# Kernel optimization log

Hardware: AMD Instinct MI355X
Metric: run time of the kernel (lower is better)

The kernel has to match this reference:

```python
import jax, jax.numpy as jnp
import numpy as np

N, E = 100000, 1600000
IN, HID, HEADS, OUT = 128, 16, 4, 64
SLOPE = 0.2  # leaky_relu negative_slope default


def setup_inputs() -> dict:
    key = jax.random.key(0)
    ks = jax.random.split(key, 12)
    s = 0.1  # xavier-ish scale
    return {
        "x": jax.random.normal(ks[0], (N, IN), jnp.float32),
        "edge_index": jax.random.randint(ks[1], (2, E), 0, N, jnp.int32),
        "W1": jax.random.normal(ks[2], (IN, HEADS * HID), jnp.float32) * s,
        "att_l1": jax.random.normal(ks[3], (1, HEADS, HID), jnp.float32) * s,
        "att_r1": jax.random.normal(ks[4], (1, HEADS, HID), jnp.float32) * s,
        "res_W1": jax.random.normal(ks[5], (IN, HEADS * HID), jnp.float32) * s,
        "b1": jnp.zeros((HEADS * HID,), jnp.float32),
        "W2": jax.random.normal(ks[6], (HEADS * HID, OUT), jnp.float32) * s,
        "att_l2": jax.random.normal(ks[7], (1, 1, OUT), jnp.float32) * s,
        "att_r2": jax.random.normal(ks[8], (1, 1, OUT), jnp.float32) * s,
        "b2": jnp.zeros((OUT,), jnp.float32),
    }


def agdn_conv(x, W, att_l, att_r, bias, res_W, src, dst):
    # x: [n, in]; W: [in, H*C]; att_*: [1, H, C]
    n = x.shape[0]
    H, C = att_l.shape[1], att_l.shape[2]
    x_lin = (x @ W).reshape(n, H, C)
    # residual: res_fc if present, else identity on x_lin (residual=True path)
    x_res = (x @ res_W) if res_W is not None else x_lin.reshape(n, H * C)
    al = jnp.sum(x_lin * att_l, axis=-1)  # [n, H]
    ar = jnp.sum(x_lin * att_r, axis=-1)  # [n, H]
    logits = jax.nn.leaky_relu(al[src] + ar[dst], SLOPE)  # [E, H]
    # segment softmax over incoming edges of each dst node
    m = jax.ops.segment_max(logits, dst, num_segments=n)
    e = jnp.exp(logits - m[dst])
    ssum = jax.ops.segment_sum(e, dst, num_segments=n)
    alpha = e / (ssum[dst] + 1e-16)  # [E, H]
    msg = x_lin[src] * alpha[:, :, None]  # [E, H, C]
    out = jax.ops.segment_sum(msg, dst, num_segments=n).reshape(n, H * C)
    return out + x_res + bias


def reference(x, edge_index, W1, att_l1, att_r1, res_W1, b1, W2, att_l2, att_r2, b2):
    src, dst = edge_index[0], edge_index[1]
    h = agdn_conv(x, W1, att_l1, att_r1, b1, res_W1, src, dst)
    h = jax.nn.elu(h)
    # last layer: heads=1, in==heads*out so res_fc is None (residual = x_lin)
    return agdn_conv(h, W2, att_l2, att_r2, b2, None, src, dst)
```

## Files before the change

kernel.cpp:

```cpp
#include <hip/hip_runtime.h>
#include <hip/hip_bf16.h>
#include <hip/hip_fp16.h>
#include <math.h>

#define NN 100000
#define EE 1600000
#define IN_DIM 128
#define HID 16
#define HEADS 4
#define D1 64
#define OUT_DIM 64
#define SLOPE 0.2f

#define NB 391
#define BCAP 5120
#define BINA_CHUNK 4096
#define BINA_BLOCKS ((EE + BINA_CHUNK - 1) / BINA_CHUNK)
#define NODE_BLOCKS ((NN + 63) / 64)
#define AGG_BLOCKS (NN / 32)

#define W1COLS 144
#define LDB1 272
#define LDB2 144

typedef __attribute__((ext_vector_type(8))) short bf16x8;
typedef __attribute__((ext_vector_type(4))) float f32x4;

__device__ __forceinline__ float leaky(float v) { return v > 0.f ? v : SLOPE * v; }
__device__ __forceinline__ unsigned short f2bf(float f) {
    __hip_bfloat16 h = __float2bfloat16(f);
    return *(unsigned short*)&h;
}
__device__ __forceinline__ __half2 u2h2(unsigned u) {
    union { unsigned u; __half2 h; } c; c.u = u; return c.h;
}
__device__ __forceinline__ bf16x8 pack8(float4 a, float4 b) {
    bf16x8 r;
    r[0] = (short)f2bf(a.x); r[1] = (short)f2bf(a.y);
    r[2] = (short)f2bf(a.z); r[3] = (short)f2bf(a.w);
    r[4] = (short)f2bf(b.x); r[5] = (short)f2bf(b.y);
    r[6] = (short)f2bf(b.z); r[7] = (short)f2bf(b.w);
    return r;
}

__global__ __launch_bounds__(256, 4) void node1_kernel(
        const float* __restrict__ x,
        const unsigned short* __restrict__ Wtb,
        const float* __restrict__ b1,
        __half* __restrict__ xlin1h,
        __half* __restrict__ acc1h,
        float* __restrict__ al1,
        float* __restrict__ ar1) {
    __shared__ char smemB[W1COLS * LDB1];
    int t = threadIdx.x;
    int base = blockIdx.x * 64;
    int wave = t >> 6, lane = t & 63;
    int quad = lane >> 4, li = lane & 15;
    int node = base + wave * 16 + li;

    uint4 breg[9];
#pragma unroll
    for (int s = 0; s < 9; s++) {
        int seg = s * 256 + t;
        breg[s] = *(const uint4*)(Wtb + (seg >> 4) * 128 + (seg & 15) * 8);
    }
    float4 xreg[8];
#pragma unroll
    for (int i = 0; i < 8; i++) xreg[i] = make_float4(0.f, 0.f, 0.f, 0.f);
    if (node < NN) {
        const float* xp = x + (size_t)node * IN_DIM + quad * 8;
#pragma unroll
        for (int kc = 0; kc < 4; kc++) {
            xreg[kc * 2]     = *(const float4*)(xp + kc * 32);
            xreg[kc * 2 + 1] = *(const float4*)(xp + kc * 32 + 4);
        }
    }
#pragma unroll
    for (int s = 0; s < 9; s++) {
        int seg = s * 256 + t;
        *(uint4*)(smemB + (seg >> 4) * LDB1 + (seg & 15) * 16) = breg[s];
    }
    __syncthreads();

    f32x4 accs[9];
#pragma unroll
    for (int nt = 0; nt < 9; nt++) accs[nt] = (f32x4){0.f, 0.f, 0.f, 0.f};
#pragma unroll
    for (int kc = 0; kc < 4; kc++) {
        bf16x8 afrag = pack8(xreg[kc * 2], xreg[kc * 2 + 1]);
        const char* brow = smemB + kc * 64 + quad * 16;
#pragma unroll
        for (int nt = 0; nt < 9; nt++) {
            bf16x8 bfrag = *(const bf16x8*)(brow + (nt * 16 + li) * LDB1);
            accs[nt] = __builtin_amdgcn_mfma_f32_16x16x32_bf16(afrag, bfrag, accs[nt], 0, 0, 0);
        }
    }

    int m0 = base + wave * 16;
#pragma unroll
    for (int nt = 0; nt < 4; nt++) {
#pragma unroll
        for (int j = 0; j < 4; j++) {
            int nd = m0 + quad * 4 + j;
            if (nd < NN) xlin1h[(size_t)nd * D1 + nt * 16 + li] = __float2half(accs[nt][j]);
        }
    }
#pragma unroll
    for (int nt = 4; nt < 8; nt++) {
        int col = (nt - 4) * 16 + li;
        float bv = b1[col];
#pragma unroll
        for (int j = 0; j < 4; j++) {
            int nd = m0 + quad * 4 + j;
            if (nd < NN) acc1h[(size_t)nd * D1 + col] = __float2half(accs[nt][j] + bv);
        }
    }
#pragma unroll
    for (int j = 0; j < 4; j++) {
        int nd = m0 + quad * 4 + j;
        if (nd < NN) {
            if (li < 4) al1[nd * HEADS + li] = accs[8][j];
            else if (li < 8) ar1[nd * HEADS + (li - 4)] = accs[8][j];
        }
    }
}

__global__ void prep_kernel(int* __restrict__ bucket_cursor,
                            const float* __restrict__ W1,
                            const float* __restrict__ resW,
                            const float* __restrict__ W2,
                            const float* __restrict__ attl1,
                            const float* __restrict__ attr1,
                            const float* __restrict__ attl2,
                            const float* __restrict__ attr2,
                            unsigned short* __restrict__ Wtb,
                            unsigned short* __restrict__ W2tb,
                            float* __restrict__ vl, float* __restrict__ vr) {
    int t = threadIdx.x;
    if (blockIdx.x == 0) {
        if (t < NB) bucket_cursor[t] = t * BCAP;
    } else if (blockIdx.x == 1) {
        for (int idx = t; idx < W1COLS * 128; idx += 512) {
            int col = idx >> 7, k = idx & 127;
            float w = 0.f;
            if (col < 64) {
                w = W1[k * 64 + col];
            } else if (col < 128) {
                w = resW[k * 64 + (col - 64)];
            } else if (col < 132) {
                int hh = col - 128;
                for (int c = 0; c < HID; c++)
                    w += W1[k * 64 + hh * HID + c] * attl1[hh * HID + c];
            } else if (col < 136) {
                int hh = col - 132;
                for (int c = 0; c < HID; c++)
                    w += W1[k * 64 + hh * HID + c] * attr1[hh * HID + c];
            }
            Wtb[idx] = f2bf(w);
        }
    } else {
        for (int idx = t; idx < 64 * 64; idx += 512) {
            int col = idx >> 6, k = idx & 63;
            W2tb[idx] = f2bf(W2[k * 64 + col]);
        }
        if (t < D1) {
            float a = 0.f, b = 0.f;
            for (int o = 0; o < OUT_DIM; o++) {
                float w = W2[t * OUT_DIM + o];
                a += w * attl2[o];
                b += w * attr2[o];
            }
            vl[t] = a; vr[t] = b;
        }
    }
}

__global__ __launch_bounds__(256) void binA_kernel(const int* __restrict__ src,
                                                   const int* __restrict__ dst,
                                                   int* __restrict__ bucket_cursor,
                                                   unsigned* __restrict__ binned) {
    __shared__ unsigned spack[BINA_CHUNK];
    __shared__ unsigned short sbkt[BINA_CHUNK];
    __shared__ int lhist[512], lscan[512], gbase[512], lcur[512];
    int t = threadIdx.x;
    lhist[t] = 0; lhist[t + 256] = 0;
    lcur[t] = 0;  lcur[t + 256] = 0;
    __syncthreads();
    int e0 = blockIdx.x * BINA_CHUNK;
    int nvalid = EE - e0; if (nvalid > BINA_CHUNK) nvalid = BINA_CHUNK;
    unsigned pk[16];
    unsigned short bk[16];
#pragma unroll
    for (int i = 0; i < 16; i++) {
        int e = e0 + t + i * 256;
        if (e < EE) {
            int d = dst[e], s = src[e];
            int b = d >> 8;
            pk[i] = ((unsigned)(d & 255) << 24) | (unsigned)s;
            bk[i] = (unsigned short)b;
            atomicAdd(&lhist[b], 1);
        } else bk[i] = 0xFFFFu;
    }
    __syncthreads();
    int c1 = lhist[t], c2 = lhist[t + 256];
    for (int off = 1; off < 512; off <<= 1) {
        int a1 = (t >= off) ? lhist[t - off] : 0;
        int a2 = (t + 256 >= off) ? lhist[t + 256 - off] : 0;
        __syncthreads();
        lhist[t] += a1; lhist[t + 256] += a2;
        __syncthreads();
    }
    lscan[t] = lhist[t] - c1;
    lscan[t + 256] = lhist[t + 256] - c2;
    if (c1) gbase[t] = atomicAdd(&bucket_cursor[t], c1);
    if (c2) gbase[t + 256] = atomicAdd(&bucket_cursor[t + 256], c2);
    __syncthreads();
#pragma unroll
    for (int i = 0; i < 16; i++) {
        if (bk[i] != 0xFFFFu) {
            int b = bk[i];
            int pos = atomicAdd(&lcur[b], 1);
            int slot = lscan[b] + pos;
            spack[slot] = pk[i];
            sbkt[slot] = (unsigned short)b;
        }
    }
    __syncthreads();
    for (int j = t; j < nvalid; j += 256) {
        int b = sbkt[j];
        int idx = gbase[b] + (j - lscan[b]);
        if (idx < (b + 1) * BCAP) binned[idx] = spack[j];
    }
}

__global__ __launch_bounds__(256) void binB_kernel(const unsigned* __restrict__ binned,
                                                   const int* __restrict__ bucket_cursor,
                                                   int* __restrict__ row_ptr,
                                                   int* __restrict__ counts,
                                                   int* __restrict__ sorted_src) {
    __shared__ int lcount[256], lrow[256], lcur[256];
    int b = blockIdx.x, t = threadIdx.x;
    int start = b * BCAP;
    int cnt = bucket_cursor[b] - start;
    if (cnt > BCAP) cnt = BCAP;
    lcount[t] = 0;
    __syncthreads();
    for (int i = t; i < cnt; i += 256) {
        atomicAdd(&lcount[binned[start + i] >> 24], 1);
    }
    __syncthreads();
    int v = lcount[t];
    lrow[t] = v;
    __syncthreads();
    for (int off = 1; off < 256; off <<= 1) {
        int a = (t >= off) ? lrow[t - off] : 0;
        __syncthreads();
        lrow[t] += a;
        __syncthreads();
    }
    int ex = lrow[t] - v;
    __syncthreads();
    lrow[t] = ex;
    lcur[t] = 0;
    int node = (b << 8) + t;
    if (node < NN) {
        row_ptr[node] = start + ex;
        counts[node] = v;
    }
    __syncthreads();
    for (int i = t; i < cnt; i += 256) {
        unsigned p = binned[start + i];
        int low = p >> 24;
        int pos = atomicAdd(&lcur[low], 1);
        sorted_src[start + lrow[low] + pos] = (int)(p & 0xFFFFFFu);
    }
}

__global__ __launch_bounds__(256) void agg1_kernel(
        const int* __restrict__ sorted_src, const int* __restrict__ row_ptr,
        const int* __restrict__ counts,
        const float* __restrict__ al1, const float* __restrict__ ar1,
        const __half* __restrict__ xlin1h, const __half* __restrict__ acc1h,
        unsigned short* __restrict__ hb,
        const float* __restrict__ vl, const float* __restrict__ vr,
        float* __restrict__ al2, float* __restrict__ ar2) {
    __shared__ __half s_alpha[4][8][65][4];
    __shared__ int    s_src[4][8][65];
    int w = threadIdx.x >> 6, lane = threadIdx.x & 63;
    int g = lane >> 3, li = lane & 7;
    int d = blockIdx.x * 32 + w * 8 + g;
    int rs = row_ptr[d];
    int deg = counts[d];
    const float4 arv = *(const float4*)(ar1 + d * 4);
    int h = li >> 1;

    int maxdeg = deg;
    maxdeg = max(maxdeg, __shfl_xor(maxdeg, 8, 64));
    maxdeg = max(maxdeg, __shfl_xor(maxdeg, 16, 64));
    maxdeg = max(maxdeg, __shfl_xor(maxdeg, 32, 64));
    bool big = maxdeg > 64;

    float s0 = 0.f, s1 = 0.f, s2 = 0.f, s3 = 0.f;
    if (!big) {
#pragma unroll
        for (int it = 0; it < 8; it++) {
            int e = li + it * 8;
            if (e < deg) {
                int s = sorted_src[rs + e];
                const float4 alv = *(const float4*)(al1 + s * 4);
                float e0 = __expf(leaky(alv.x + arv.x));
                float e1 = __expf(leaky(alv.y + arv.y));
                float e2 = __expf(leaky(alv.z + arv.z));
                float e3 = __expf(leaky(alv.w + arv.w));
                s0 += e0; s1 += e1; s2 += e2; s3 += e3;
                __half2 h01 = __floats2half2_rn(e0, e1);
                __half2 h23 = __floats2half2_rn(e2, e3);
                *(uint2*)&s_alpha[w][g][e][0] =
                    make_uint2(*(unsigned*)&h01, *(unsigned*)&h23);
                s_src[w][g][e] = s;
            }
        }
    } else {
        for (int e = li; e < deg; e += 8) {
            int s = sorted_src[rs + e];
            const float4 alv = *(const float4*)(al1 + s * 4);
            s0 += __expf(leaky(alv.x + arv.x));
            s1 += __expf(leaky(alv.y + arv.y));
            s2 += __expf(leaky(alv.z + arv.z));
            s3 += __expf(leaky(alv.w + arv.w));
        }
    }
#pragma unroll
    for (int off = 1; off < 8; off <<= 1) {
        s0 += __shfl_xor(s0, off, 64);
        s1 += __shfl_xor(s1, off, 64);
        s2 += __shfl_xor(s2, off, 64);
        s3 += __shfl_xor(s3, off, 64);
    }
    float inv0 = 0.f, inv1 = 0.f, inv2 = 0.f, inv3 = 0.f;
    if (deg > 0) {
        inv0 = 1.f / (s0 + 1e-16f); inv1 = 1.f / (s1 + 1e-16f);
        inv2 = 1.f / (s2 + 1e-16f); inv3 = 1.f / (s3 + 1e-16f);
    }
    float invh = (h == 0) ? inv0 : (h == 1) ? inv1 : (h == 2) ? inv2 : inv3;
    __half2 invh2 = __floats2half2_rn(invh, invh);

    __half2 a01 = __floats2half2_rn(0.f, 0.f);
    __half2 a23 = a01, a45 = a01, a67 = a01;
    float fb0=0.f, fb1=0.f, fb2=0.f, fb3=0.f, fb4=0.f, fb5=0.f, fb6=0.f, fb7=0.f;
    if (!big) {
        for (int i0 = 0; i0 < maxdeg; i0 += 4) {
            int ss[4]; __half ah[4]; uint4 uu[4];
#pragma unroll
            for (int j = 0; j < 4; j++) {
                int i = i0 + j;
                ah[j] = __float2half(0.f);
                ss[j] = 0;
                if (i < deg) { ss[j] = s_src[w][g][i]; ah[j] = s_alpha[w][g][i][h]; }
            }
#pragma unroll
            for (int j = 0; j < 4; j++) {
                int i = i0 + j;
                uu[j] = make_uint4(0u, 0u, 0u, 0u);
                if (i < deg) uu[j] = *(const uint4*)(xlin1h + (size_t)ss[j] * D1 + li * 8);
            }
#pragma unroll
            for (int j = 0; j < 4; j++) {
                __half2 a2 = __hmul2(__half2half2(ah[j]), invh2);
                a01 = __hfma2(a2, u2h2(uu[j].x), a01);
                a23 = __hfma2(a2, u2h2(uu[j].y), a23);
                a45 = __hfma2(a2, u2h2(uu[j].z), a45);
                a67 = __hfma2(a2, u2h2(uu[j].w), a67);
            }
        }
    } else {
        float arh = (h == 0) ? arv.x : (h == 1) ? arv.y : (h == 2) ? arv.z : arv.w;
        for (int i = 0; i < deg; i++) {
            int s = sorted_src[rs + i];
            const float4 alv = *(const float4*)(al1 + s * 4);
            float lv = (h == 0) ? alv.x : (h == 1) ? alv.y : (h == 2) ? alv.z : alv.w;
            float a = __expf(leaky(lv + arh)) * invh;
            uint4 u = *(const uint4*)(xlin1h + (size_t)s * D1 + li * 8);
            float2 x01 = __half22float2(u2h2(u.x));
            float2 x23 = __half22float2(u2h2(u.y));
            float2 x45 = __half22float2(u2h2(u.z));
            float2 x67 = __half22float2(u2h2(u.w));
            fb0 += a * x01.x; fb1 += a * x01.y; fb2 += a * x23.x; fb3 += a * x23.y;
            fb4 += a * x45.x; fb5 += a * x45.y; fb6 += a * x67.x; fb7 += a * x67.y;
        }
    }
    float c0, c1, c2, c3, c4, c5, c6, c7;
    { float2 tv;
      tv = __half22float2(a01); c0 = tv.x + fb0; c1 = tv.y + fb1;
      tv = __half22float2(a23); c2 = tv.x + fb2; c3 = tv.y + fb3;
      tv = __half22float2(a45); c4 = tv.x + fb4; c5 = tv.y + fb5;
      tv = __half22float2(a67); c6 = tv.x + fb6; c7 = tv.y + fb7; }
    uint4 rres = *(const uint4*)(acc1h + (size_t)d * D1 + li * 8);
    { float2 tv;
      tv = __half22float2(u2h2(rres.x)); c0 += tv.x; c1 += tv.y;
      tv = __half22float2(u2h2(rres.y)); c2 += tv.x; c3 += tv.y;
      tv = __half22float2(u2h2(rres.z)); c4 += tv.x; c5 += tv.y;
      tv = __half22float2(u2h2(rres.w)); c6 += tv.x; c7 += tv.y; }
    c0 = c0 > 0.f ? c0 : (__expf(c0) - 1.f);
    c1 = c1 > 0.f ? c1 : (__expf(c1) - 1.f);
    c2 = c2 > 0.f ? c2 : (__expf(c2) - 1.f);
    c3 = c3 > 0.f ? c3 : (__expf(c3) - 1.f);
    c4 = c4 > 0.f ? c4 : (__expf(c4) - 1.f);
    c5 = c5 > 0.f ? c5 : (__expf(c5) - 1.f);
    c6 = c6 > 0.f ? c6 : (__expf(c6) - 1.f);
    c7 = c7 > 0.f ? c7 : (__expf(c7) - 1.f);
    union { unsigned short us[8]; uint4 u4; } hw;
    hw.us[0] = f2bf(c0); hw.us[1] = f2bf(c1); hw.us[2] = f2bf(c2); hw.us[3] = f2bf(c3);
    hw.us[4] = f2bf(c4); hw.us[5] = f2bf(c5); hw.us[6] = f2bf(c6); hw.us[7] = f2bf(c7);
    *(uint4*)(hb + (size_t)d * D1 + li * 8) = hw.u4;
    const float4 vla = *(const float4*)(vl + li * 8);
    const float4 vlb = *(const float4*)(vl + li * 8 + 4);
    const float4 vra = *(const float4*)(vr + li * 8);
    const float4 vrb = *(const float4*)(vr + li * 8 + 4);
    float pl = c0 * vla.x + c1 * vla.y + c2 * vla.z + c3 * vla.w
             + c4 * vlb.x + c5 * vlb.y + c6 * vlb.z + c7 * vlb.w;
    float pr = c0 * vra.x + c1 * vra.y + c2 * vra.z + c3 * vra.w
             + c4 * vrb.x + c5 * vrb.y + c6 * vrb.z + c7 * vrb.w;
#pragma unroll
    for (int off = 1; off < 8; off <<= 1) {
        pl += __shfl_xor(pl, off, 64);
        pr += __shfl_xor(pr, off, 64);
    }
    if (li == 0) { al2[d] = pl; ar2[d] = pr; }
}

__global__ __launch_bounds__(256) void node2_kernel(
        const unsigned short* __restrict__ hb,
        const unsigned short* __restrict__ W2tb,
        __half* __restrict__ xlin2h) {
    __shared__ char smemB[64 * LDB2];
    int t = threadIdx.x;
    int base = blockIdx.x * 64;
    int wave = t >> 6, lane = t & 63;
    int quad = lane >> 4, li = lane & 15;
    int node = base + wave * 16 + li;

    uint4 breg[2];
#pragma unroll
    for (int s = 0; s < 2; s++) {
        int seg = s * 256 + t;
        breg[s] = *(const uint4*)(W2tb + (seg >> 3) * 64 + (seg & 7) * 8);
    }
    bf16x8 afr[2];
#pragma unroll
    for (int kc = 0; kc < 2; kc++)
#pragma unroll
        for (int i = 0; i < 8; i++) afr[kc][i] = 0;
    if (node < NN) {
        afr[0] = *(const bf16x8*)(hb + (size_t)node * D1 + quad * 8);
        afr[1] = *(const bf16x8*)(hb + (size_t)node * D1 + 32 + quad * 8);
    }
#pragma unroll
    for (int s = 0; s < 2; s++) {
        int seg = s * 256 + t;
        *(uint4*)(smemB + (seg >> 3) * LDB2 + (seg & 7) * 16) = breg[s];
    }
    __syncthreads();

    f32x4 accs[4];
#pragma unroll
    for (int nt = 0; nt < 4; nt++) accs[nt] = (f32x4){0.f, 0.f, 0.f, 0.f};
#pragma unroll
    for (int kc = 0; kc < 2; kc++) {
        const char* brow = smemB + kc * 64 + quad * 16;
#pragma unroll
        for (int nt = 0; nt < 4; nt++) {
            bf16x8 bfrag = *(const bf16x8*)(brow + (nt * 16 + li) * LDB2);
            accs[nt] = __builtin_amdgcn_mfma_f32_16x16x32_bf16(afr[kc], bfrag, accs[nt], 0, 0, 0);
        }
    }

    int m0 = base + wave * 16;
#pragma unroll
    for (int nt = 0; nt < 4; nt++) {
        int col = nt * 16 + li;
#pragma unroll
        for (int j = 0; j < 4; j++) {
            int nd = m0 + quad * 4 + j;
            if (nd < NN) xlin2h[(size_t)nd * OUT_DIM + col] = __float2half(accs[nt][j]);
        }
    }
}

__global__ __launch_bounds__(256) void agg2_kernel(
        const int* __restrict__ sorted_src, const int* __restrict__ row_ptr,
        const int* __restrict__ counts,
        const float* __restrict__ al2, const float* __restrict__ ar2,
        const __half* __restrict__ xlin2h, const float* __restrict__ b2,
        float* __restrict__ out) {
    __shared__ __half s_alpha[4][8][65];
    __shared__ int    s_src[4][8][65];
    int w = threadIdx.x >> 6, lane = threadIdx.x & 63;
    int g = lane >> 3, li = lane & 7;
    int d = blockIdx.x * 32 + w * 8 + g;
    int rs = row_ptr[d];
    int deg = counts[d];
    float ard = ar2[d];

    int maxdeg = deg;
    maxdeg = max(maxdeg, __shfl_xor(maxdeg, 8, 64));
    maxdeg = max(maxdeg, __shfl_xor(maxdeg, 16, 64));
    maxdeg = max(maxdeg, __shfl_xor(maxdeg, 32, 64));
    bool big = maxdeg > 64;

    float ssum = 0.f;
    if (!big) {
#pragma unroll
        for (int it = 0; it < 8; it++) {
            int e = li + it * 8;
            if (e < deg) {
                int s = sorted_src[rs + e];
                float ex = __expf(leaky(al2[s] + ard));
                ssum += ex;
                s_alpha[w][g][e] = __float2half(ex);
                s_src[w][g][e] = s;
            }
        }
    } else {
        for (int e = li; e < deg; e += 8) {
            int s = sorted_src[rs + e];
            ssum += __expf(leaky(al2[s] + ard));
        }
    }
#pragma unroll
    for (int off = 1; off < 8; off <<= 1) ssum += __shfl_xor(ssum, off, 64);
    float inv = (deg > 0) ? 1.f / (ssum + 1e-16f) : 0.f;
    __half2 inv2h = __floats2half2_rn(inv, inv);

    __half2 a01 = __floats2half2_rn(0.f, 0.f);
    __half2 a23 = a01, a45 = a01, a67 = a01;
    float fb0=0.f, fb1=0.f, fb2=0.f, fb3=0.f, fb4=0.f, fb5=0.f, fb6=0.f, fb7=0.f;
    if (!big) {
        for (int i0 = 0; i0 < maxdeg; i0 += 4) {
            int ss[4]; __half ah[4]; uint4 uu[4];
#pragma unroll
            for (int j = 0; j < 4; j++) {
                int i = i0 + j;
                ah[j] = __float2half(0.f);
                ss[j] = 0;
                if (i < deg) { ss[j] = s_src[w][g][i]; ah[j] = s_alpha[w][g][i]; }
            }
#pragma unroll
            for (int j = 0; j < 4; j++) {
                int i = i0 + j;
                uu[j] = make_uint4(0u, 0u, 0u, 0u);
                if (i < deg) uu[j] = *(const uint4*)(xlin2h + (size_t)ss[j] * OUT_DIM + li * 8);
            }
#pragma unroll
            for (int j = 0; j < 4; j++) {
                __half2 a2 = __hmul2(__half2half2(ah[j]), inv2h);
                a01 = __hfma2(a2, u2h2(uu[j].x), a01);
                a23 = __hfma2(a2, u2h2(uu[j].y), a23);
                a45 = __hfma2(a2, u2h2(uu[j].z), a45);
                a67 = __hfma2(a2, u2h2(uu[j].w), a67);
            }
        }
    } else {
        for (int i = 0; i < deg; i++) {
            int s = sorted_src[rs + i];
            float a = __expf(leaky(al2[s] + ard)) * inv;
            uint4 u = *(const uint4*)(xlin2h + (size_t)s * OUT_DIM + li * 8);
            float2 x01 = __half22float2(u2h2(u.x));
            float2 x23 = __half22float2(u2h2(u.y));
            float2 x45 = __half22float2(u2h2(u.z));
            float2 x67 = __half22float2(u2h2(u.w));
            fb0 += a * x01.x; fb1 += a * x01.y; fb2 += a * x23.x; fb3 += a * x23.y;
            fb4 += a * x45.x; fb5 += a * x45.y; fb6 += a * x67.x; fb7 += a * x67.y;
        }
    }
    float c0, c1, c2, c3, c4, c5, c6, c7;
    { float2 tv;
      tv = __half22float2(a01); c0 = tv.x + fb0; c1 = tv.y + fb1;
      tv = __half22float2(a23); c2 = tv.x + fb2; c3 = tv.y + fb3;
      tv = __half22float2(a45); c4 = tv.x + fb4; c5 = tv.y + fb5;
      tv = __half22float2(a67); c6 = tv.x + fb6; c7 = tv.y + fb7; }
    uint4 own = *(const uint4*)(xlin2h + (size_t)d * OUT_DIM + li * 8);
    { float2 tv;
      tv = __half22float2(u2h2(own.x)); c0 += tv.x; c1 += tv.y;
      tv = __half22float2(u2h2(own.y)); c2 += tv.x; c3 += tv.y;
      tv = __half22float2(u2h2(own.z)); c4 += tv.x; c5 += tv.y;
      tv = __half22float2(u2h2(own.w)); c6 += tv.x; c7 += tv.y; }
    const float4 bva = *(const float4*)(b2 + li * 8);
    const float4 bvb = *(const float4*)(b2 + li * 8 + 4);
    c0 += bva.x; c1 += bva.y; c2 += bva.z; c3 += bva.w;
    c4 += bvb.x; c5 += bvb.y; c6 += bvb.z; c7 += bvb.w;
    float* p = out + (size_t)d * OUT_DIM + li * 8;
    *(float4*)p = make_float4(c0, c1, c2, c3);
    *(float4*)(p + 4) = make_float4(c4, c5, c6, c7);
}

extern "C" void kernel_launch(void* const* d_in, const int* in_sizes, int n_in,
                              void* d_out, int out_size, void* d_ws, size_t ws_size,
                              hipStream_t stream) {
    const float* x     = (const float*)d_in[0];
    const int*   eidx  = (const int*)d_in[1];
    const float* W1    = (const float*)d_in[2];
    const float* attl1 = (const float*)d_in[3];
    const float* attr1 = (const float*)d_in[4];
    const float* resW1 = (const float*)d_in[5];
    const float* b1    = (const float*)d_in[6];
    const float* W2    = (const float*)d_in[7];
    const float* attl2 = (const float*)d_in[8];
    const float* attr2 = (const float*)d_in[9];
    const float* b2    = (const float*)d_in[10];

    const int* src = eidx;
    const int* dst = eidx + EE;

    __half* xlin1h = (__half*)d_ws;
    __half* acc1h  = xlin1h + (size_t)NN * D1;
    unsigned short* hb = (unsigned short*)(acc1h + (size_t)NN * D1);
    float* al1   = (float*)(hb + (size_t)NN * D1);
    float* ar1   = al1 + (size_t)NN * HEADS;
    float* al2   = ar1 + (size_t)NN * HEADS;
    float* ar2   = al2 + NN;
    float* vl    = ar2 + NN;
    float* vr    = vl + D1;
    unsigned short* Wtb  = (unsigned short*)(vr + D1);
    unsigned short* W2tb = Wtb + W1COLS * 128;
    int* counts        = (int*)(W2tb + 64 * 64);
    int* row_ptr       = counts + NN;
    int* bucket_cursor = row_ptr + NN;
    int* sorted_src    = bucket_cursor + 512;
    unsigned* binned = (unsigned*)d_out;
    __half* xlin2h = xlin1h;

    float* out = (float*)d_out;

    prep_kernel<<<3, 512, 0, stream>>>(bucket_cursor, W1, resW1, W2,
                                       attl1, attr1, attl2, attr2,
                                       Wtb, W2tb, vl, vr);
    binA_kernel<<<BINA_BLOCKS, 256, 0, stream>>>(src, dst, bucket_cursor, binned);
    node1_kernel<<<NODE_BLOCKS, 256, 0, stream>>>(x, Wtb, b1,
                                                  xlin1h, acc1h, al1, ar1);
    binB_kernel<<<NB, 256, 0, stream>>>(binned, bucket_cursor,
                                        row_ptr, counts, sorted_src);

    agg1_kernel<<<AGG_BLOCKS, 256, 0, stream>>>(sorted_src, row_ptr, counts,
                                                al1, ar1, xlin1h, acc1h, hb,
                                                vl, vr, al2, ar2);

    node2_kernel<<<NODE_BLOCKS, 256, 0, stream>>>(hb, W2tb, xlin2h);
    agg2_kernel<<<AGG_BLOCKS, 256, 0, stream>>>(sorted_src, row_ptr, counts,
                                                al2, ar2, xlin2h, b2, out);
}
```

Before: 258.1 us.

## Aggregate before layer-2 projection, fuse binning with node1, unroll gathers by eight

Layer 2 now aggregates the 64-dim ELU output h directly and applies W2 afterward, using linearity: the sum of alpha·h plus h is multiplied by W2 once per node. The layer-2 attention logits still come from the precomputed vl/vr projections. The binA and node1 kernels are merged into one launch that picks its role by block index, so the two independent stages can overlap. The gather loops in both aggregation kernels are unrolled from 4 to 8 for more memory-level parallelism. This adds an extra rounding step through half/bf16 storage of the aggregated sum, which may change numerics, and the deeper unroll raises register use.

```diff
diff --git a/kernel.cpp b/kernel.cpp
--- a/kernel.cpp
+++ b/kernel.cpp
@@ -41,88 +41,6 @@
     r[4] = (short)f2bf(b.x); r[5] = (short)f2bf(b.y);
     r[6] = (short)f2bf(b.z); r[7] = (short)f2bf(b.w);
     return r;
-}
-
-__global__ __launch_bounds__(256, 4) void node1_kernel(
-        const float* __restrict__ x,
-        const unsigned short* __restrict__ Wtb,
-        const float* __restrict__ b1,
-        __half* __restrict__ xlin1h,
-        __half* __restrict__ acc1h,
-        float* __restrict__ al1,
-        float* __restrict__ ar1) {
-    __shared__ char smemB[W1COLS * LDB1];
-    int t = threadIdx.x;
-    int base = blockIdx.x * 64;
-    int wave = t >> 6, lane = t & 63;
-    int quad = lane >> 4, li = lane & 15;
-    int node = base + wave * 16 + li;
-
-    uint4 breg[9];
-#pragma unroll
-    for (int s = 0; s < 9; s++) {
-        int seg = s * 256 + t;
-        breg[s] = *(const uint4*)(Wtb + (seg >> 4) * 128 + (seg & 15) * 8);
-    }
-    float4 xreg[8];
-#pragma unroll
-    for (int i = 0; i < 8; i++) xreg[i] = make_float4(0.f, 0.f, 0.f, 0.f);
-    if (node < NN) {
-        const float* xp = x + (size_t)node * IN_DIM + quad * 8;
-#pragma unroll
-        for (int kc = 0; kc < 4; kc++) {
-            xreg[kc * 2]     = *(const float4*)(xp + kc * 32);
-            xreg[kc * 2 + 1] = *(const float4*)(xp + kc * 32 + 4);
-        }
-    }
-#pragma unroll
-    for (int s = 0; s < 9; s++) {
-        int seg = s * 256 + t;
-        *(uint4*)(smemB + (seg >> 4) * LDB1 + (seg & 15) * 16) = breg[s];
-    }
-    __syncthreads();
-
-    f32x4 accs[9];
-#pragma unroll
-    for (int nt = 0; nt < 9; nt++) accs[nt] = (f32x4){0.f, 0.f, 0.f, 0.f};
-#pragma unroll
-    for (int kc = 0; kc < 4; kc++) {
-        bf16x8 afrag = pack8(xreg[kc * 2], xreg[kc * 2 + 1]);
-        const char* brow = smemB + kc * 64 + quad * 16;
-#pragma unroll
-        for (int nt = 0; nt < 9; nt++) {
-            bf16x8 bfrag = *(const bf16x8*)(brow + (nt * 16 + li) * LDB1);
-            accs[nt] = __builtin_amdgcn_mfma_f32_16x16x32_bf16(afrag, bfrag, accs[nt], 0, 0, 0);
-        }
-    }
-
-    int m0 = base + wave * 16;
-#pragma unroll
-    for (int nt = 0; nt < 4; nt++) {
-#pragma unroll
-        for (int j = 0; j < 4; j++) {
-            int nd = m0 + quad * 4 + j;
-            if (nd < NN) xlin1h[(size_t)nd * D1 + nt * 16 + li] = __float2half(accs[nt][j]);
-        }
-    }
-#pragma unroll
-    for (int nt = 4; nt < 8; nt++) {
-        int col = (nt - 4) * 16 + li;
-        float bv = b1[col];
-#pragma unroll
-        for (int j = 0; j < 4; j++) {
-            int nd = m0 + quad * 4 + j;
-            if (nd < NN) acc1h[(size_t)nd * D1 + col] = __float2half(accs[nt][j] + bv);
-        }
-    }
-#pragma unroll
-    for (int j = 0; j < 4; j++) {
-        int nd = m0 + quad * 4 + j;
-        if (nd < NN) {
-            if (li < 4) al1[nd * HEADS + li] = accs[8][j];
-            else if (li < 8) ar1[nd * HEADS + (li - 4)] = accs[8][j];
-        }
-    }
 }
 
 __global__ void prep_kernel(int* __restrict__ bucket_cursor,
@@ -175,18 +93,20 @@
     }
 }
 
-__global__ __launch_bounds__(256) void binA_kernel(const int* __restrict__ src,
-                                                   const int* __restrict__ dst,
-                                                   int* __restrict__ bucket_cursor,
-                                                   unsigned* __restrict__ binned) {
-    __shared__ unsigned spack[BINA_CHUNK];
-    __shared__ unsigned short sbkt[BINA_CHUNK];
-    __shared__ int lhist[512], lscan[512], gbase[512], lcur[512];
+__device__ __forceinline__ void binA_body(char* smem, int bid,
+        const int* __restrict__ src, const int* __restrict__ dst,
+        int* __restrict__ bucket_cursor, unsigned* __restrict__ binned) {
+    unsigned* spack = (unsigned*)smem;
+    unsigned short* sbkt = (unsigned short*)(smem + 16384);
+    int* lhist = (int*)(smem + 24576);
+    int* lscan = lhist + 512;
+    int* gbase = lscan + 512;
+    int* lcur  = gbase + 512;
     int t = threadIdx.x;
     lhist[t] = 0; lhist[t + 256] = 0;
     lcur[t] = 0;  lcur[t + 256] = 0;
     __syncthreads();
-    int e0 = blockIdx.x * BINA_CHUNK;
+    int e0 = bid * BINA_CHUNK;
     int nvalid = EE - e0; if (nvalid > BINA_CHUNK) nvalid = BINA_CHUNK;
     unsigned pk[16];
     unsigned short bk[16];
@@ -231,6 +151,98 @@
         int idx = gbase[b] + (j - lscan[b]);
         if (idx < (b + 1) * BCAP) binned[idx] = spack[j];
     }
+}
+
+__device__ __forceinline__ void node1_body(char* smemB, int bid,
+        const float* __restrict__ x, const unsigned short* __restrict__ Wtb,
+        const float* __restrict__ b1, __half* __restrict__ xlin1h,
+        __half* __restrict__ acc1h, float* __restrict__ al1,
+        float* __restrict__ ar1) {
+    int t = threadIdx.x;
+    int base = bid * 64;
+    int wave = t >> 6, lane = t & 63;
+    int quad = lane >> 4, li = lane & 15;
+    int node = base + wave * 16 + li;
+
+    uint4 breg[9];
+#pragma unroll
+    for (int s = 0; s < 9; s++) {
+        int seg = s * 256 + t;
+        breg[s] = *(const uint4*)(Wtb + (seg >> 4) * 128 + (seg & 15) * 8);
+    }
+    float4 xreg[8];
+#pragma unroll
+    for (int i = 0; i < 8; i++) xreg[i] = make_float4(0.f, 0.f, 0.f, 0.f);
+    if (node < NN) {
+        const float* xp = x + (size_t)node * IN_DIM + quad * 8;
+#pragma unroll
+        for (int kc = 0; kc < 4; kc++) {
+            xreg[kc * 2]     = *(const float4*)(xp + kc * 32);
+            xreg[kc * 2 + 1] = *(const float4*)(xp + kc * 32 + 4);
+        }
+    }
+#pragma unroll
+    for (int s = 0; s < 9; s++) {
+        int seg = s * 256 + t;
+        *(uint4*)(smemB + (seg >> 4) * LDB1 + (seg & 15) * 16) = breg[s];
+    }
+    __syncthreads();
+
+    f32x4 accs[9];
+#pragma unroll
+    for (int nt = 0; nt < 9; nt++) accs[nt] = (f32x4){0.f, 0.f, 0.f, 0.f};
+#pragma unroll
+    for (int kc = 0; kc < 4; kc++) {
+        bf16x8 afrag = pack8(xreg[kc * 2], xreg[kc * 2 + 1]);
+        const char* brow = smemB + kc * 64 + quad * 16;
+#pragma unroll
+        for (int nt = 0; nt < 9; nt++) {
+            bf16x8 bfrag = *(const bf16x8*)(brow + (nt * 16 + li) * LDB1);
+            accs[nt] = __builtin_amdgcn_mfma_f32_16x16x32_bf16(afrag, bfrag, accs[nt], 0, 0, 0);
+        }
+    }
+
+    int m0 = base + wave * 16;
+#pragma unroll
+    for (int nt = 0; nt < 4; nt++) {
+#pragma unroll
+        for (int j = 0; j < 4; j++) {
+            int nd = m0 + quad * 4 + j;
+            if (nd < NN) xlin1h[(size_t)nd * D1 + nt * 16 + li] = __float2half(accs[nt][j]);
+        }
+    }
+#pragma unroll
+    for (int nt = 4; nt < 8; nt++) {
+        int col = (nt - 4) * 16 + li;
+        float bv = b1[col];
+#pragma unroll
+        for (int j = 0; j < 4; j++) {
+            int nd = m0 + quad * 4 + j;
+            if (nd < NN) acc1h[(size_t)nd * D1 + col] = __float2half(accs[nt][j] + bv);
+        }
+    }
+#pragma unroll
+    for (int j = 0; j < 4; j++) {
+        int nd = m0 + quad * 4 + j;
+        if (nd < NN) {
+            if (li < 4) al1[nd * HEADS + li] = accs[8][j];
+            else if (li < 8) ar1[nd * HEADS + (li - 4)] = accs[8][j];
+        }
+    }
+}
+
+__global__ __launch_bounds__(256, 4) void fusedA_kernel(
+        const int* __restrict__ src, const int* __restrict__ dst,
+        int* __restrict__ bucket_cursor, unsigned* __restrict__ binned,
+        const float* __restrict__ x, const unsigned short* __restrict__ Wtb,
+        const float* __restrict__ b1, __half* __restrict__ xlin1h,
+        __half* __restrict__ acc1h, float* __restrict__ al1,
+        float* __restrict__ ar1) {
+    __shared__ __align__(16) char smem[W1COLS * LDB1];
+    if (blockIdx.x < BINA_BLOCKS)
+        binA_body(smem, blockIdx.x, src, dst, bucket_cursor, binned);
+    else
+        node1_body(smem, blockIdx.x - BINA_BLOCKS, x, Wtb, b1, xlin1h, acc1h, al1, ar1);
 }
 
 __global__ __launch_bounds__(256) void binB_kernel(const unsigned* __restrict__ binned,
@@ -281,7 +293,7 @@
         const int* __restrict__ counts,
         const float* __restrict__ al1, const float* __restrict__ ar1,
         const __half* __restrict__ xlin1h, const __half* __restrict__ acc1h,
-        unsigned short* __restrict__ hb,
+        __half* __restrict__ hh,
         const float* __restrict__ vl, const float* __restrict__ vr,
         float* __restrict__ al2, float* __restrict__ ar2) {
     __shared__ __half s_alpha[4][8][65][4];
@@ -349,23 +361,23 @@
     __half2 a23 = a01, a45 = a01, a67 = a01;
     float fb0=0.f, fb1=0.f, fb2=0.f, fb3=0.f, fb4=0.f, fb5=0.f, fb6=0.f, fb7=0.f;
     if (!big) {
-        for (int i0 = 0; i0 < maxdeg; i0 += 4) {
-            int ss[4]; __half ah[4]; uint4 uu[4];
-#pragma unroll
-            for (int j = 0; j < 4; j++) {
+        for (int i0 = 0; i0 < maxdeg; i0 += 8) {
+            int ss[8]; __half ah[8]; uint4 uu[8];
+#pragma unroll
+            for (int j = 0; j < 8; j++) {
                 int i = i0 + j;
-                ah[j] = __float2half(0.f);
-                ss[j] = 0;
-                if (i < deg) { ss[j] = s_src[w][g][i]; ah[j] = s_alpha[w][g][i][h]; }
-            }
-#pragma unroll
-            for (int j = 0; j < 4; j++) {
+                bool v = i < deg;
+                ss[j] = v ? s_src[w][g][i] : 0;
+                ah[j] = v ? s_alpha[w][g][i][h] : __float2half(0.f);
+            }
+#pragma unroll
+            for (int j = 0; j < 8; j++) {
                 int i = i0 + j;
                 uu[j] = make_uint4(0u, 0u, 0u, 0u);
                 if (i < deg) uu[j] = *(const uint4*)(xlin1h + (size_t)ss[j] * D1 + li * 8);
             }
 #pragma unroll
-            for (int j = 0; j < 4; j++) {
+            for (int j = 0; j < 8; j++) {
                 __half2 a2 = __hmul2(__half2half2(ah[j]), invh2);
                 a01 = __hfma2(a2, u2h2(uu[j].x), a01);
                 a23 = __hfma2(a2, u2h2(uu[j].y), a23);
@@ -409,10 +421,13 @@
     c5 = c5 > 0.f ? c5 : (__expf(c5) - 1.f);
     c6 = c6 > 0.f ? c6 : (__expf(c6) - 1.f);
     c7 = c7 > 0.f ? c7 : (__expf(c7) - 1.f);
-    union { unsigned short us[8]; uint4 u4; } hw;
-    hw.us[0] = f2bf(c0); hw.us[1] = f2bf(c1); hw.us[2] = f2bf(c2); hw.us[3] = f2bf(c3);
-    hw.us[4] = f2bf(c4); hw.us[5] = f2bf(c5); hw.us[6] = f2bf(c6); hw.us[7] = f2bf(c7);
-    *(uint4*)(hb + (size_t)d * D1 + li * 8) = hw.u4;
+    __half2 o01 = __floats2half2_rn(c0, c1);
+    __half2 o23 = __floats2half2_rn(c2, c3);
+    __half2 o45 = __floats2half2_rn(c4, c5);
+    __half2 o67 = __floats2half2_rn(c6, c7);
+    uint4 hv = make_uint4(*(unsigned*)&o01, *(unsigned*)&o23,
+                          *(unsigned*)&o45, *(unsigned*)&o67);
+    *(uint4*)(hh + (size_t)d * D1 + li * 8) = hv;
     const float4 vla = *(const float4*)(vl + li * 8);
     const float4 vlb = *(const float4*)(vl + li * 8 + 4);
     const float4 vra = *(const float4*)(vr + li * 8);
@@ -429,70 +444,12 @@
     if (li == 0) { al2[d] = pl; ar2[d] = pr; }
 }
 
-__global__ __launch_bounds__(256) void node2_kernel(
-        const unsigned short* __restrict__ hb,
-        const unsigned short* __restrict__ W2tb,
-        __half* __restrict__ xlin2h) {
-    __shared__ char smemB[64 * LDB2];
-    int t = threadIdx.x;
-    int base = blockIdx.x * 64;
-    int wave = t >> 6, lane = t & 63;
-    int quad = lane >> 4, li = lane & 15;
-    int node = base + wave * 16 + li;
-
-    uint4 breg[2];
-#pragma unroll
-    for (int s = 0; s < 2; s++) {
-        int seg = s * 256 + t;
-        breg[s] = *(const uint4*)(W2tb + (seg >> 3) * 64 + (seg & 7) * 8);
-    }
-    bf16x8 afr[2];
-#pragma unroll
-    for (int kc = 0; kc < 2; kc++)
-#pragma unroll
-        for (int i = 0; i < 8; i++) afr[kc][i] = 0;
-    if (node < NN) {
-        afr[0] = *(const bf16x8*)(hb + (size_t)node * D1 + quad * 8);
-        afr[1] = *(const bf16x8*)(hb + (size_t)node * D1 + 32 + quad * 8);
-    }
-#pragma unroll
-    for (int s = 0; s < 2; s++) {
-        int seg = s * 256 + t;
-        *(uint4*)(smemB + (seg >> 3) * LDB2 + (seg & 7) * 16) = breg[s];
-    }
-    __syncthreads();
-
-    f32x4 accs[4];
-#pragma unroll
-    for (int nt = 0; nt < 4; nt++) accs[nt] = (f32x4){0.f, 0.f, 0.f, 0.f};
-#pragma unroll
-    for (int kc = 0; kc < 2; kc++) {
-        const char* brow = smemB + kc * 64 + quad * 16;
-#pragma unroll
-        for (int nt = 0; nt < 4; nt++) {
-            bf16x8 bfrag = *(const bf16x8*)(brow + (nt * 16 + li) * LDB2);
-            accs[nt] = __builtin_amdgcn_mfma_f32_16x16x32_bf16(afr[kc], bfrag, accs[nt], 0, 0, 0);
-        }
-    }
-
-    int m0 = base + wave * 16;
-#pragma unroll
-    for (int nt = 0; nt < 4; nt++) {
-        int col = nt * 16 + li;
-#pragma unroll
-        for (int j = 0; j < 4; j++) {
-            int nd = m0 + quad * 4 + j;
-            if (nd < NN) xlin2h[(size_t)nd * OUT_DIM + col] = __float2half(accs[nt][j]);
-        }
-    }
-}
-
 __global__ __launch_bounds__(256) void agg2_kernel(
         const int* __restrict__ sorted_src, const int* __restrict__ row_ptr,
         const int* __restrict__ counts,
         const float* __restrict__ al2, const float* __restrict__ ar2,
-        const __half* __restrict__ xlin2h, const float* __restrict__ b2,
-        float* __restrict__ out) {
+        const __half* __restrict__ hh,
+        unsigned short* __restrict__ hsum) {
     __shared__ __half s_alpha[4][8][65];
     __shared__ int    s_src[4][8][65];
     int w = threadIdx.x >> 6, lane = threadIdx.x & 63;
@@ -536,23 +493,23 @@
     __half2 a23 = a01, a45 = a01, a67 = a01;
     float fb0=0.f, fb1=0.f, fb2=0.f, fb3=0.f, fb4=0.f, fb5=0.f, fb6=0.f, fb7=0.f;
     if (!big) {
-        for (int i0 = 0; i0 < maxdeg; i0 += 4) {
-            int ss[4]; __half ah[4]; uint4 uu[4];
-#pragma unroll
-            for (int j = 0; j < 4; j++) {
+        for (int i0 = 0; i0 < maxdeg; i0 += 8) {
+            int ss[8]; __half ah[8]; uint4 uu[8];
+#pragma unroll
+            for (int j = 0; j < 8; j++) {
                 int i = i0 + j;
-                ah[j] = __float2half(0.f);
-                ss[j] = 0;
-                if (i < deg) { ss[j] = s_src[w][g][i]; ah[j] = s_alpha[w][g][i]; }
-            }
-#pragma unroll
-            for (int j = 0; j < 4; j++) {
+                bool v = i < deg;
+                ss[j] = v ? s_src[w][g][i] : 0;
+                ah[j] = v ? s_alpha[w][g][i] : __float2half(0.f);
+            }
+#pragma unroll
+            for (int j = 0; j < 8; j++) {
                 int i = i0 + j;
                 uu[j] = make_uint4(0u, 0u, 0u, 0u);
-                if (i < deg) uu[j] = *(const uint4*)(xlin2h + (size_t)ss[j] * OUT_DIM + li * 8);
-            }
-#pragma unroll
-            for (int j = 0; j < 4; j++) {
+                if (i < deg) uu[j] = *(const uint4*)(hh + (size_t)ss[j] * D1 + li * 8);
+            }
+#pragma unroll
+            for (int j = 0; j < 8; j++) {
                 __half2 a2 = __hmul2(__half2half2(ah[j]), inv2h);
                 a01 = __hfma2(a2, u2h2(uu[j].x), a01);
                 a23 = __hfma2(a2, u2h2(uu[j].y), a23);
@@ -564,7 +521,7 @@
         for (int i = 0; i < deg; i++) {
             int s = sorted_src[rs + i];
             float a = __expf(leaky(al2[s] + ard)) * inv;
-            uint4 u = *(const uint4*)(xlin2h + (size_t)s * OUT_DIM + li * 8);
+            uint4 u = *(const uint4*)(hh + (size_t)s * D1 + li * 8);
             float2 x01 = __half22float2(u2h2(u.x));
             float2 x23 = __half22float2(u2h2(u.y));
             float2 x45 = __half22float2(u2h2(u.z));
@@ -579,19 +536,76 @@
       tv = __half22float2(a23); c2 = tv.x + fb2; c3 = tv.y + fb3;
       tv = __half22float2(a45); c4 = tv.x + fb4; c5 = tv.y + fb5;
       tv = __half22float2(a67); c6 = tv.x + fb6; c7 = tv.y + fb7; }
-    uint4 own = *(const uint4*)(xlin2h + (size_t)d * OUT_DIM + li * 8);
+    uint4 own = *(const uint4*)(hh + (size_t)d * D1 + li * 8);
     { float2 tv;
       tv = __half22float2(u2h2(own.x)); c0 += tv.x; c1 += tv.y;
       tv = __half22float2(u2h2(own.y)); c2 += tv.x; c3 += tv.y;
       tv = __half22float2(u2h2(own.z)); c4 += tv.x; c5 += tv.y;
       tv = __half22float2(u2h2(own.w)); c6 += tv.x; c7 += tv.y; }
-    const float4 bva = *(const float4*)(b2 + li * 8);
-    const float4 bvb = *(const float4*)(b2 + li * 8 + 4);
-    c0 += bva.x; c1 += bva.y; c2 += bva.z; c3 += bva.w;
-    c4 += bvb.x; c5 += bvb.y; c6 += bvb.z; c7 += bvb.w;
-    float* p = out + (size_t)d * OUT_DIM + li * 8;
-    *(float4*)p = make_float4(c0, c1, c2, c3);
-    *(float4*)(p + 4) = make_float4(c4, c5, c6, c7);
+    union { unsigned short us[8]; uint4 u4; } hw;
+    hw.us[0] = f2bf(c0); hw.us[1] = f2bf(c1); hw.us[2] = f2bf(c2); hw.us[3] = f2bf(c3);
+    hw.us[4] = f2bf(c4); hw.us[5] = f2bf(c5); hw.us[6] = f2bf(c6); hw.us[7] = f2bf(c7);
+    *(uint4*)(hsum + (size_t)d * D1 + li * 8) = hw.u4;
+}
+
+__global__ __launch_bounds__(256) void node3_kernel(
+        const unsigned short* __restrict__ hsum,
+        const unsigned short* __restrict__ W2tb,
+        const float* __restrict__ b2,
+        float* __restrict__ out) {
+    __shared__ char smemB[64 * LDB2];
+    int t = threadIdx.x;
+    int base = blockIdx.x * 64;
+    int wave = t >> 6, lane = t & 63;
+    int quad = lane >> 4, li = lane & 15;
+    int node = base + wave * 16 + li;
+
+    uint4 breg[2];
+#pragma unroll
+    for (int s = 0; s < 2; s++) {
+        int seg = s * 256 + t;
+        breg[s] = *(const uint4*)(W2tb + (seg >> 3) * 64 + (seg & 7) * 8);
+    }
+    bf16x8 afr[2];
+#pragma unroll
+    for (int kc = 0; kc < 2; kc++)
+#pragma unroll
+        for (int i = 0; i < 8; i++) afr[kc][i] = 0;
+    if (node < NN) {
+        afr[0] = *(const bf16x8*)(hsum + (size_t)node * D1 + quad * 8);
+        afr[1] = *(const bf16x8*)(hsum + (size_t)node * D1 + 32 + quad * 8);
+    }
+#pragma unroll
+    for (int s = 0; s < 2; s++) {
+        int seg = s * 256 + t;
+        *(uint4*)(smemB + (seg >> 3) * LDB2 + (seg & 7) * 16) = breg[s];
+    }
+    __syncthreads();
+
+    f32x4 accs[4];
+#pragma unroll
+    for (int nt = 0; nt < 4; nt++) accs[nt] = (f32x4){0.f, 0.f, 0.f, 0.f};
+#pragma unroll
+    for (int kc = 0; kc < 2; kc++) {
+        const char* brow = smemB + kc * 64 + quad * 16;
+#pragma unroll
+        for (int nt = 0; nt < 4; nt++) {
+            bf16x8 bfrag = *(const bf16x8*)(brow + (nt * 16 + li) * LDB2);
+            accs[nt] = __builtin_amdgcn_mfma_f32_16x16x32_bf16(afr[kc], bfrag, accs[nt], 0, 0, 0);
+        }
+    }
+
+    int m0 = base + wave * 16;
+#pragma unroll
+    for (int nt = 0; nt < 4; nt++) {
+        int col = nt * 16 + li;
+        float bv = b2[col];
+#pragma unroll
+        for (int j = 0; j < 4; j++) {
+            int nd = m0 + quad * 4 + j;
+            if (nd < NN) out[(size_t)nd * OUT_DIM + col] = accs[nt][j] + bv;
+        }
+    }
 }
 
 extern "C" void kernel_launch(void* const* d_in, const int* in_sizes, int n_in,
@@ -614,8 +628,9 @@
 
     __half* xlin1h = (__half*)d_ws;
     __half* acc1h  = xlin1h + (size_t)NN * D1;
-    unsigned short* hb = (unsigned short*)(acc1h + (size_t)NN * D1);
-    float* al1   = (float*)(hb + (size_t)NN * D1);
+    __half* hh     = acc1h + (size_t)NN * D1;
+    unsigned short* hsum = (unsigned short*)(hh + (size_t)NN * D1);
+    float* al1   = (float*)(hsum + (size_t)NN * D1);
     float* ar1   = al1 + (size_t)NN * HEADS;
     float* al2   = ar1 + (size_t)NN * HEADS;
     float* ar2   = al2 + NN;
@@ -628,24 +643,23 @@
     int* bucket_cursor = row_ptr + NN;
     int* sorted_src    = bucket_cursor + 512;
     unsigned* binned = (unsigned*)d_out;
-    __half* xlin2h = xlin1h;
 
     float* out = (float*)d_out;
 
     prep_kernel<<<3, 512, 0, stream>>>(bucket_cursor, W1, resW1, W2,
                                        attl1, attr1, attl2, attr2,
                                        Wtb, W2tb, vl, vr);
-    binA_kernel<<<BINA_BLOCKS, 256, 0, stream>>>(src, dst, bucket_cursor, binned);
-    node1_kernel<<<NODE_BLOCKS, 256, 0, stream>>>(x, Wtb, b1,
-                                                  xlin1h, acc1h, al1, ar1);
+    fusedA_kernel<<<BINA_BLOCKS + NODE_BLOCKS, 256, 0, stream>>>(
+        src, dst, bucket_cursor, binned,
+        x, Wtb, b1, xlin1h, acc1h, al1, ar1);
     binB_kernel<<<NB, 256, 0, stream>>>(binned, bucket_cursor,
                                         row_ptr, counts, sorted_src);
 
     agg1_kernel<<<AGG_BLOCKS, 256, 0, stream>>>(sorted_src, row_ptr, counts,
-                                                al1, ar1, xlin1h, acc1h, hb,
+                                                al1, ar1, xlin1h, acc1h, hh,
                                                 vl, vr, al2, ar2);
 
-    node2_kernel<<<NODE_BLOCKS, 256, 0, stream>>>(hb, W2tb, xlin2h);
     agg2_kernel<<<AGG_BLOCKS, 256, 0, stream>>>(sorted_src, row_ptr, counts,
-                                                al2, ar2, xlin2h, b2, out);
-}
+                                                al2, ar2, hh, hsum);
+    node3_kernel<<<NODE_BLOCKS, 256, 0, stream>>>(hsum, W2tb, b2, out);
+}
```

New measurement: 245.2 us. 5.0% less time.
